# Optimization experiments

Measured on AMD Instinct MI355X. Metric: run time of the kernel, lower is better.

## Reference

```python
import jax, jax.numpy as jnp
import numpy as np

N_EMBD = 1024
N_HEAD = 16
HEAD_SIZE = N_EMBD // N_HEAD  # 64
ROT = HEAD_SIZE // 2          # 32 (int(head_size * 0.5))
BASE = 10000.0


def rotate_half(x):
    x1, x2 = x[..., : x.shape[-1] // 2], x[..., x.shape[-1] // 2 :]
    return jnp.concatenate((-x2, x1), axis=-1)


def rope_tables(T, dtype=jnp.float32):
    inv_freq = 1.0 / (BASE ** (jnp.arange(0, ROT, 2, dtype=jnp.float32) / ROT))
    t = jnp.arange(T, dtype=jnp.float32)
    freqs = jnp.einsum('i,j->ij', t, inv_freq)  # [T, ROT//2]
    emb = jnp.concatenate((freqs, freqs), axis=-1)  # [T, ROT]
    return jnp.cos(emb).astype(dtype), jnp.sin(emb).astype(dtype)


def setup_inputs() -> dict:
    key = jax.random.key(0)
    ks = jax.random.split(key, 9)
    B, T, C = 2, 2048, N_EMBD
    s = 1.0 / np.sqrt(C)
    inp = {
        'x': jax.random.normal(ks[0], (B, T, C), dtype=jnp.float32),
        'Wq': jax.random.normal(ks[1], (C, C), dtype=jnp.float32) * s,
        'bq': jnp.zeros((C,), dtype=jnp.float32),
        'Wk': jax.random.normal(ks[2], (C, C), dtype=jnp.float32) * s,
        'bk': jnp.zeros((C,), dtype=jnp.float32),
        'Wv': jax.random.normal(ks[3], (C, C), dtype=jnp.float32) * s,
        'bv': jnp.zeros((C,), dtype=jnp.float32),
        'Wo': jax.random.normal(ks[4], (C, C), dtype=jnp.float32) * s,
        'bo': jnp.zeros((C,), dtype=jnp.float32),
    }
    return inp


def reference(x, Wq, bq, Wk, bk, Wv, bv, Wo, bo):
    B, T, C = x.shape
    H, D = N_HEAD, HEAD_SIZE

    def proj(W, b):
        return (x @ W + b).reshape(B, T, H, D).transpose(0, 2, 1, 3)  # [B,H,T,D]

    q, k, v = proj(Wq, bq), proj(Wk, bk), proj(Wv, bv)

    q_rot, q_pass = q[..., :ROT], q[..., ROT:]
    k_rot, k_pass = k[..., :ROT], k[..., ROT:]
    cos, sin = rope_tables(T, x.dtype)  # [T, ROT]
    q_rot = q_rot * cos + rotate_half(q_rot) * sin
    k_rot = k_rot * cos + rotate_half(k_rot) * sin
    q = jnp.concatenate((q_rot, q_pass), axis=-1)
    k = jnp.concatenate((k_rot, k_pass), axis=-1)

    scale = 1.0 / np.sqrt(D)
    att = jnp.einsum('bhqd,bhkd->bhqk', q, k) * scale  # [B,H,T,T]
    causal = jnp.tril(jnp.ones((T, T), dtype=bool))
    att = jnp.where(causal, att, -jnp.inf)
    att = jax.nn.softmax(att, axis=-1)
    out = jnp.einsum('bhqk,bhkd->bhqd', att, v)  # [B,H,T,D]
    out = out.transpose(0, 2, 1, 3).reshape(B, T, C)
    return out @ Wo + bo
```

## Files before the change

### kernel.cpp

```cpp
#include <hip/hip_runtime.h>
#include <cstdint>
#include <cstddef>
#include <math.h>

typedef _Float16 half8 __attribute__((ext_vector_type(8)));
typedef _Float16 half4 __attribute__((ext_vector_type(4)));
typedef float f32x4 __attribute__((ext_vector_type(4)));
typedef float f32x16 __attribute__((ext_vector_type(16)));
typedef unsigned int uint2v __attribute__((ext_vector_type(2)));

#define NB  2
#define NT  2048
#define NC  1024
#define NH  16
#define ND  64

__device__ __forceinline__ void gload_lds16(const _Float16* g, _Float16* l) {
  __builtin_amdgcn_global_load_lds((const __attribute__((address_space(1))) void*)g,
                                   (__attribute__((address_space(3))) void*)l, 16, 0, 0);
}

__device__ __forceinline__ uint2v plswap(unsigned a, unsigned b) {
  return __builtin_amdgcn_permlane32_swap(a, b, false, false);
}

__global__ void k_cvt_x(const float* __restrict__ x, _Float16* __restrict__ xh) {
  const int n4 = (4096 * 1024) / 4;
  int i = blockIdx.x * 256 + threadIdx.x;
  for (; i < n4; i += 2048 * 256) {
    float4 v = ((const float4*)x)[i];
    half4 h = { (_Float16)v.x, (_Float16)v.y, (_Float16)v.z, (_Float16)v.w };
    ((half4*)xh)[i] = h;
  }
}

__global__ void k_tw(const float* __restrict__ W0, const float* __restrict__ W1,
                     const float* __restrict__ W2, const float* __restrict__ W3,
                     _Float16* __restrict__ WT) {
  const float* W = (blockIdx.z == 0) ? W0 : (blockIdx.z == 1) ? W1 : (blockIdx.z == 2) ? W2 : W3;
  _Float16* out = WT + ((size_t)blockIdx.z << 20);
  __shared__ float t[32][33];
  const int x0 = blockIdx.x * 32;
  const int y0 = blockIdx.y * 32;
  const int tx = threadIdx.x, ty = threadIdx.y;
#pragma unroll
  for (int r = 0; r < 4; ++r)
    t[ty + 8 * r][tx] = W[(size_t)(y0 + ty + 8 * r) * 1024 + x0 + tx];
  __syncthreads();
#pragma unroll
  for (int r = 0; r < 4; ++r)
    out[(size_t)(x0 + ty + 8 * r) * 1024 + y0 + tx] = (_Float16)t[tx][ty + 8 * r];
}

__device__ __forceinline__ void gemm_mainloop(const _Float16* __restrict__ A,
                                              const _Float16* __restrict__ Bmat,
                                              int m0, int n0,
                                              _Float16* As, _Float16* Bs,
                                              f32x4 acc[4][4]) {
  const int tid = threadIdx.x;
  const int lane = tid & 63;
  const int wid = tid >> 6;
  const int wm = wid >> 1, wn = wid & 1;
  const int c16 = lane & 15, rg = lane >> 4;

  for (int k0 = 0; k0 < 1024; k0 += 64) {
    __syncthreads();
#pragma unroll
    for (int i = 0; i < 4; ++i) {
      int e = (i * 256 + tid) * 8;
      int row = e >> 6;
      int chunk = (e & 63) >> 3;
      int scol = ((chunk ^ (row & 7)) << 3);
      gload_lds16(A + (size_t)(m0 + row) * 1024 + k0 + scol,
                  As + (size_t)(i * 256 + (wid << 6)) * 8);
      gload_lds16(Bmat + (size_t)(n0 + row) * 1024 + k0 + scol,
                  Bs + (size_t)(i * 256 + (wid << 6)) * 8);
    }
    __syncthreads();
#pragma unroll
    for (int kk = 0; kk < 2; ++kk) {
      half8 af[4], bfr[4];
#pragma unroll
      for (int mi = 0; mi < 4; ++mi) {
        int row = (wm << 6) + (mi << 4) + c16;
        int chunk = (kk << 2) + rg;
        af[mi] = *(const half8*)&As[(row << 6) + ((chunk ^ (row & 7)) << 3)];
      }
#pragma unroll
      for (int ni = 0; ni < 4; ++ni) {
        int row = (wn << 6) + (ni << 4) + c16;
        int chunk = (kk << 2) + rg;
        bfr[ni] = *(const half8*)&Bs[(row << 6) + ((chunk ^ (row & 7)) << 3)];
      }
#pragma unroll
      for (int mi = 0; mi < 4; ++mi)
#pragma unroll
        for (int ni = 0; ni < 4; ++ni)
          acc[mi][ni] = __builtin_amdgcn_mfma_f32_16x16x32_f16(af[mi], bfr[ni], acc[mi][ni], 0, 0, 0);
    }
  }
}

__global__ __launch_bounds__(256, 2) void k_qkv(const _Float16* __restrict__ xh,
                                                const _Float16* __restrict__ WT,
                                                const float* __restrict__ bq,
                                                const float* __restrict__ bk,
                                                const float* __restrict__ bv,
                                                _Float16* __restrict__ Qh,
                                                _Float16* __restrict__ Kh,
                                                _Float16* __restrict__ VT) {
  __shared__ __align__(16) _Float16 As[128 * 64];
  __shared__ __align__(16) _Float16 Bs[128 * 64];
  f32x4 acc[4][4];
#pragma unroll
  for (int i = 0; i < 4; ++i)
#pragma unroll
    for (int j = 0; j < 4; ++j) acc[i][j] = (f32x4){0.f, 0.f, 0.f, 0.f};

  const int m0 = blockIdx.y * 128;
  const int ng = blockIdx.x * 128;
  const int p = ng >> 10;
  const int n0 = ng & 1023;
  gemm_mainloop(xh, WT + ((size_t)p << 20), m0, n0, As, Bs, acc);

  const int tid = threadIdx.x, lane = tid & 63, wid = tid >> 6;
  const int wm = wid >> 1, wn = wid & 1, c16 = lane & 15, rg = lane >> 4;
  const float* bias = (p == 0) ? bq : (p == 1) ? bk : bv;
  const int nw = n0 + (wn << 6);
  const int head = nw >> 6;
  float bi[4];
#pragma unroll
  for (int ni = 0; ni < 4; ++ni) bi[ni] = bias[nw + (ni << 4) + c16];

  if (p == 2) {
#pragma unroll
    for (int mi = 0; mi < 4; ++mi) {
      int m = m0 + (wm << 6) + (mi << 4) + (rg << 2);
      int b = m >> 11, t0 = m & 2047;
#pragma unroll
      for (int ni = 0; ni < 4; ++ni) {
        half4 hv;
#pragma unroll
        for (int r = 0; r < 4; ++r) hv[r] = (_Float16)(acc[mi][ni][r] + bi[ni]);
        size_t base = ((size_t)(b * NH + head) * ND + (ni << 4) + c16) * NT + t0;
        *(half4*)&VT[base] = hv;
      }
    }
    return;
  }

  _Float16* Out = (p == 0) ? Qh : Kh;
  const float invf = exp2f((float)c16 * -0.8304820237218405f);
  const float qscale = (p == 0) ? 0.18033688011112042f : 1.0f;

#pragma unroll
  for (int mi = 0; mi < 4; ++mi) {
#pragma unroll
    for (int r = 0; r < 4; ++r) {
      int m = m0 + (wm << 6) + (mi << 4) + (rg << 2) + r;
      int b = m >> 11, t = m & 2047;
      float v0 = acc[mi][0][r] + bi[0];
      float v1 = acc[mi][1][r] + bi[1];
      float v2 = acc[mi][2][r] + bi[2];
      float v3 = acc[mi][3][r] + bi[3];
      {
        float th = (float)t * invf;
        float sn, cs;
        sincosf(th, &sn, &cs);
        float nx = v0 * cs - v1 * sn;
        v1 = v1 * cs + v0 * sn;
        v0 = nx;
      }
      size_t base = ((size_t)(b * NH + head) * NT + t) * ND;
      Out[base + 0 + c16]  = (_Float16)(v0 * qscale);
      Out[base + 16 + c16] = (_Float16)(v1 * qscale);
      Out[base + 32 + c16] = (_Float16)(v2 * qscale);
      Out[base + 48 + c16] = (_Float16)(v3 * qscale);
    }
  }
}

__global__ __launch_bounds__(256, 2) void k_attn(const _Float16* __restrict__ Qh,
                                                 const _Float16* __restrict__ Kh,
                                                 const _Float16* __restrict__ VT,
                                                 _Float16* __restrict__ Oh) {
  const int lin = blockIdx.x;
  const int xcd = lin & 7;
  const int w = lin >> 3;
  const int bh = (xcd << 2) | (w & 3);
  const int tile = 15 - (w >> 2);

  const int tid = threadIdx.x, lane = tid & 63, wid = tid >> 6;
  const int q31 = lane & 31, hi = lane >> 5;
  const size_t hb = (size_t)bh * NT * ND;
  const _Float16* Qp = Qh + hb;
  const _Float16* Kp = Kh + hb;
  const _Float16* Vp = VT + hb;
  const int b = bh >> 4, h = bh & 15;

  const int q0w = (tile << 7) + (wid << 5);
  const int qg = q0w + q31;
  const int end = q0w + 32;

  half8 qf[4];
#pragma unroll
  for (int c = 0; c < 4; ++c)
    qf[c] = *(const half8*)&Qp[(size_t)qg * ND + (c << 4) + (hi << 3)];

  f32x16 oacc0, oacc1, lacc;
#pragma unroll
  for (int r = 0; r < 16; ++r) { oacc0[r] = 0.f; oacc1[r] = 0.f; lacc[r] = 0.f; }
  float m = -INFINITY;

  half8 kA[4], kB[4], vfr[4];

#define LOADK(dst, ktv) do {                                                    \
    const _Float16* kp_ = Kp + (size_t)((ktv) + q31) * ND + (hi << 3);          \
    dst[0] = *(const half8*)(kp_);                                              \
    dst[1] = *(const half8*)(kp_ + 16);                                         \
    dst[2] = *(const half8*)(kp_ + 32);                                         \
    dst[3] = *(const half8*)(kp_ + 48);                                         \
  } while (0)

#define LOADV(ktv) do {                                                         \
    _Pragma("unroll")                                                           \
    for (int dh = 0; dh < 2; ++dh)                                              \
      _Pragma("unroll")                                                         \
      for (int ks = 0; ks < 2; ++ks)                                            \
        vfr[dh * 2 + ks] = *(const half8*)&Vp[(size_t)((dh << 5) + q31) * NT    \
                                              + (ktv) + (ks << 4) + (hi << 3)]; \
  } while (0)

#define BODY(kb, ktc) do {                                                      \
    f32x16 s;                                                                   \
    _Pragma("unroll")                                                           \
    for (int r = 0; r < 16; ++r) s[r] = 0.f;                                    \
    __builtin_amdgcn_s_setprio(1);                                              \
    _Pragma("unroll")                                                           \
    for (int c = 0; c < 4; ++c)                                                 \
      s = __builtin_amdgcn_mfma_f32_32x32x16_f16(kb[c], qf[c], s, 0, 0, 0);     \
    __builtin_amdgcn_s_setprio(0);                                              \
    if ((ktc) + 31 > q0w) {      \
      int rel = qg - (ktc) - (hi << 2);                                         \
      _Pragma("unroll")                                                         \
      for (int r = 0; r < 16; ++r) {                                            \
        int crow = (r & 3) + ((r >> 2) << 3);                                   \
        if (crow > rel) s[r] = -INFINITY;                                       \
      }                                                                         \
    }                                                                           \
       \
    float t8[8];                                                                \
    _Pragma("unroll")                                                           \
    for (int r = 0; r < 8; ++r) t8[r] = fmaxf(s[r], s[r + 8]);                  \
    _Pragma("unroll")                                                           \
    for (int r = 0; r < 4; ++r) t8[r] = fmaxf(t8[r], t8[r + 4]);                \
    float pm = fmaxf(fmaxf(t8[0], t8[1]), fmaxf(t8[2], t8[3]));                 \
    pm = fmaxf(pm, __shfl_xor(pm, 32));                                         \
    if (!__all(pm <= m + 11.54f)) {                 \
      float mn = fmaxf(m, pm);                                                  \
      float corr = exp2f(m - mn);                                               \
      m = mn;                                                                   \
      _Pragma("unroll")                                                         \
      for (int r = 0; r < 16; ++r) {                                            \
        oacc0[r] *= corr; oacc1[r] *= corr; lacc[r] *= corr;                    \
      }                                                                         \
    }                                                                           \
    _Pragma("unroll")                                                           \
    for (int r = 0; r < 16; ++r) {                                              \
      float pv = exp2f(s[r] - m);                                               \
      s[r] = pv; lacc[r] += pv;                                                 \
    }                                                                           \
     \
    unsigned pw0 = __builtin_bit_cast(unsigned, __builtin_amdgcn_cvt_pkrtz(s[0], s[1]));   \
    unsigned pw1 = __builtin_bit_cast(unsigned, __builtin_amdgcn_cvt_pkrtz(s[2], s[3]));   \
    unsigned pw2 = __builtin_bit_cast(unsigned, __builtin_amdgcn_cvt_pkrtz(s[4], s[5]));   \
    unsigned pw3 = __builtin_bit_cast(unsigned, __builtin_amdgcn_cvt_pkrtz(s[6], s[7]));   \
    unsigned pw4 = __builtin_bit_cast(unsigned, __builtin_amdgcn_cvt_pkrtz(s[8], s[9]));   \
    unsigned pw5 = __builtin_bit_cast(unsigned, __builtin_amdgcn_cvt_pkrtz(s[10], s[11])); \
    unsigned pw6 = __builtin_bit_cast(unsigned, __builtin_amdgcn_cvt_pkrtz(s[12], s[13])); \
    unsigned pw7 = __builtin_bit_cast(unsigned, __builtin_amdgcn_cvt_pkrtz(s[14], s[15])); \
    uint2v rA0 = plswap(pw0, pw2);   \
    uint2v rA1 = plswap(pw1, pw3);                      \
    uint2v rB0 = plswap(pw4, pw6);                      \
    uint2v rB1 = plswap(pw5, pw7);                      \
    uint4 ua, ub;                                                               \
    ua.x = rA0[0]; ua.y = rA1[0]; ua.z = rA0[1]; ua.w = rA1[1];                 \
    ub.x = rB0[0]; ub.y = rB1[0]; ub.z = rB0[1]; ub.w = rB1[1];                 \
    half8 pa0 = __builtin_bit_cast(half8, ua);                                  \
    half8 pa1 = __builtin_bit_cast(half8, ub);                                  \
    __builtin_amdgcn_s_setprio(1);                                              \
    oacc0 = __builtin_amdgcn_mfma_f32_32x32x16_f16(vfr[0], pa0, oacc0, 0, 0, 0); \
    oacc0 = __builtin_amdgcn_mfma_f32_32x32x16_f16(vfr[1], pa1, oacc0, 0, 0, 0); \
    oacc1 = __builtin_amdgcn_mfma_f32_32x32x16_f16(vfr[2], pa0, oacc1, 0, 0, 0); \
    oacc1 = __builtin_amdgcn_mfma_f32_32x32x16_f16(vfr[3], pa1, oacc1, 0, 0, 0); \
    __builtin_amdgcn_s_setprio(0);                                              \
  } while (0)

  int kt = 0;
  LOADK(kA, 0);
  for (;;) {
    LOADV(kt);
    if (kt + 32 < end) LOADK(kB, kt + 32);
    __builtin_amdgcn_sched_barrier(0);
    BODY(kA, kt);
    kt += 32;
    if (kt >= end) break;
    LOADV(kt);
    if (kt + 32 < end) LOADK(kA, kt + 32);
    __builtin_amdgcn_sched_barrier(0);
    BODY(kB, kt);
    kt += 32;
    if (kt >= end) break;
  }
#undef LOADK
#undef LOADV
#undef BODY

  float l8[8];
#pragma unroll
  for (int r = 0; r < 8; ++r) l8[r] = lacc[r] + lacc[r + 8];
#pragma unroll
  for (int r = 0; r < 4; ++r) l8[r] = l8[r] + l8[r + 4];
  float ls = (l8[0] + l8[1]) + (l8[2] + l8[3]);
  ls += __shfl_xor(ls, 32);
  float il = 1.f / ls;
  size_t obase = ((size_t)b * NT + qg) * NC + h * ND;
#pragma unroll
  for (int g = 0; g < 4; ++g) {
    int d0 = (g << 3) + (hi << 2);
    half4 h4, h5;
#pragma unroll
    for (int r = 0; r < 4; ++r) {
      h4[r] = (_Float16)(oacc0[(g << 2) + r] * il);
      h5[r] = (_Float16)(oacc1[(g << 2) + r] * il);
    }
    *(half4*)&Oh[obase + d0] = h4;
    *(half4*)&Oh[obase + 32 + d0] = h5;
  }
}

__global__ __launch_bounds__(256, 2) void k_out(const _Float16* __restrict__ Oh,
                                                const _Float16* __restrict__ WoT,
                                                const float* __restrict__ bo,
                                                float* __restrict__ out) {
  __shared__ __align__(16) _Float16 As[128 * 64];
  __shared__ __align__(16) _Float16 Bs[128 * 64];
  f32x4 acc[4][4];
#pragma unroll
  for (int i = 0; i < 4; ++i)
#pragma unroll
    for (int j = 0; j < 4; ++j) acc[i][j] = (f32x4){0.f, 0.f, 0.f, 0.f};

  const int m0 = blockIdx.y * 128;
  const int n0 = blockIdx.x * 128;
  gemm_mainloop(Oh, WoT, m0, n0, As, Bs, acc);

  const int tid = threadIdx.x, lane = tid & 63, wid = tid >> 6;
  const int wm = wid >> 1, wn = wid & 1, c16 = lane & 15, rg = lane >> 4;
  float bi[4];
#pragma unroll
  for (int ni = 0; ni < 4; ++ni) bi[ni] = bo[n0 + (wn << 6) + (ni << 4) + c16];
#pragma unroll
  for (int mi = 0; mi < 4; ++mi) {
#pragma unroll
    for (int r = 0; r < 4; ++r) {
      int m = m0 + (wm << 6) + (mi << 4) + (rg << 2) + r;
#pragma unroll
      for (int ni = 0; ni < 4; ++ni) {
        int n = n0 + (wn << 6) + (ni << 4) + c16;
        out[(size_t)m * NC + n] = acc[mi][ni][r] + bi[ni];
      }
    }
  }
}

extern "C" void kernel_launch(void* const* d_in, const int* in_sizes, int n_in,
                              void* d_out, int out_size, void* d_ws, size_t ws_size,
                              hipStream_t stream) {
  const float* x  = (const float*)d_in[0];
  const float* Wq = (const float*)d_in[1];
  const float* bq = (const float*)d_in[2];
  const float* Wk = (const float*)d_in[3];
  const float* bk = (const float*)d_in[4];
  const float* Wv = (const float*)d_in[5];
  const float* bv = (const float*)d_in[6];
  const float* Wo = (const float*)d_in[7];
  const float* bo = (const float*)d_in[8];
  float* out = (float*)d_out;

  char* ws = (char*)d_ws;
  _Float16* xh = (_Float16*)ws;
  _Float16* WT = (_Float16*)(ws + (8ull << 20));
  _Float16* Qh = (_Float16*)(ws + (16ull << 20));
  _Float16* Kh = (_Float16*)(ws + (24ull << 20));
  _Float16* Vt = (_Float16*)(ws + (32ull << 20));
  _Float16* Oh = (_Float16*)(ws + (40ull << 20));

  k_cvt_x<<<2048, 256, 0, stream>>>(x, xh);
  k_tw<<<dim3(32, 32, 4), dim3(32, 8), 0, stream>>>(Wq, Wk, Wv, Wo, WT);
  k_qkv<<<dim3(24, 32), 256, 0, stream>>>(xh, WT, bq, bk, bv, Qh, Kh, Vt);
  k_attn<<<512, 256, 0, stream>>>(Qh, Kh, Vt, Oh);
  k_out<<<dim3(8, 32), 256, 0, stream>>>(Oh, WT + (3ull << 20), bo, out);
}
```

Before: 151.9 us.

## Split attention KV range across two waves per query tile and merge via LDS

Each attention block now owns one 32-row query tile with two waves, each wave processing half of the causal key range (split-K flash attention), then merging partial max, sum and output through shared memory. The grid grows from 512 blocks of 4 waves to 2048 blocks of 2 waves, and the row-sum accumulator is halved by pre-adding pairs. The aim is to shorten the longest per-wave key loop and balance the causal triangle across more independent work units. In exchange it adds an LDS round trip, a block barrier and a rescale merge, and it drops the previous XCD-aware block mapping.

```diff
diff --git a/kernel.cpp b/kernel.cpp
--- a/kernel.cpp
+++ b/kernel.cpp
@@ -180,15 +180,13 @@
   }
 }
 
-__global__ __launch_bounds__(256, 2) void k_attn(const _Float16* __restrict__ Qh,
+__global__ __launch_bounds__(128, 4) void k_attn(const _Float16* __restrict__ Qh,
                                                  const _Float16* __restrict__ Kh,
                                                  const _Float16* __restrict__ VT,
                                                  _Float16* __restrict__ Oh) {
   const int lin = blockIdx.x;
-  const int xcd = lin & 7;
-  const int w = lin >> 3;
-  const int bh = (xcd << 2) | (w & 3);
-  const int tile = 15 - (w >> 2);
+  const int bh = lin & 31;
+  const int g = 63 - (lin >> 5);
 
   const int tid = threadIdx.x, lane = tid & 63, wid = tid >> 6;
   const int q31 = lane & 31, hi = lane >> 5;
@@ -198,18 +196,27 @@
   const _Float16* Vp = VT + hb;
   const int b = bh >> 4, h = bh & 15;
 
-  const int q0w = (tile << 7) + (wid << 5);
+  __shared__ float Osh[32][65];
+  __shared__ float msh[32], lsh[32];
+
+  const int q0w = g << 5;
   const int qg = q0w + q31;
-  const int end = q0w + 32;
+  const int n = g + 1;
+  const int nh2 = (n + 1) >> 1;
+  const int kt0   = (wid == 0) ? 0 : (nh2 << 5);
+  const int ktend = (wid == 0) ? (nh2 << 5) : (n << 5);
 
   half8 qf[4];
 #pragma unroll
   for (int c = 0; c < 4; ++c)
     qf[c] = *(const half8*)&Qp[(size_t)qg * ND + (c << 4) + (hi << 3)];
 
-  f32x16 oacc0, oacc1, lacc;
-#pragma unroll
-  for (int r = 0; r < 16; ++r) { oacc0[r] = 0.f; oacc1[r] = 0.f; lacc[r] = 0.f; }
+  f32x16 oacc0, oacc1;
+#pragma unroll
+  for (int r = 0; r < 16; ++r) { oacc0[r] = 0.f; oacc1[r] = 0.f; }
+  float lacc[8];
+#pragma unroll
+  for (int r = 0; r < 8; ++r) lacc[r] = 0.f;
   float m = -INFINITY;
 
   half8 kA[4], kB[4], vfr[4];
@@ -240,7 +247,7 @@
     for (int c = 0; c < 4; ++c)                                                 \
       s = __builtin_amdgcn_mfma_f32_32x32x16_f16(kb[c], qf[c], s, 0, 0, 0);     \
     __builtin_amdgcn_s_setprio(0);                                              \
-    if ((ktc) + 31 > q0w) {      \
+    if ((ktc) + 31 > q0w) {       \
       int rel = qg - (ktc) - (hi << 2);                                         \
       _Pragma("unroll")                                                         \
       for (int r = 0; r < 16; ++r) {                                            \
@@ -248,7 +255,7 @@
         if (crow > rel) s[r] = -INFINITY;                                       \
       }                                                                         \
     }                                                                           \
-       \
+                       \
     float t8[8];                                                                \
     _Pragma("unroll")                                                           \
     for (int r = 0; r < 8; ++r) t8[r] = fmaxf(s[r], s[r + 8]);                  \
@@ -261,16 +268,18 @@
       float corr = exp2f(m - mn);                                               \
       m = mn;                                                                   \
       _Pragma("unroll")                                                         \
-      for (int r = 0; r < 16; ++r) {                                            \
-        oacc0[r] *= corr; oacc1[r] *= corr; lacc[r] *= corr;                    \
-      }                                                                         \
+      for (int r = 0; r < 16; ++r) { oacc0[r] *= corr; oacc1[r] *= corr; }      \
+      _Pragma("unroll")                                                         \
+      for (int r = 0; r < 8; ++r) lacc[r] *= corr;                              \
     }                                                                           \
     _Pragma("unroll")                                                           \
     for (int r = 0; r < 16; ++r) {                                              \
       float pv = exp2f(s[r] - m);                                               \
-      s[r] = pv; lacc[r] += pv;                                                 \
+      s[r] = pv;                                                                \
     }                                                                           \
-     \
+    _Pragma("unroll")                                                           \
+    for (int r = 0; r < 8; ++r) lacc[r] += s[r] + s[r + 8];                     \
+      \
     unsigned pw0 = __builtin_bit_cast(unsigned, __builtin_amdgcn_cvt_pkrtz(s[0], s[1]));   \
     unsigned pw1 = __builtin_bit_cast(unsigned, __builtin_amdgcn_cvt_pkrtz(s[2], s[3]));   \
     unsigned pw2 = __builtin_bit_cast(unsigned, __builtin_amdgcn_cvt_pkrtz(s[4], s[5]));   \
@@ -279,10 +288,10 @@
     unsigned pw5 = __builtin_bit_cast(unsigned, __builtin_amdgcn_cvt_pkrtz(s[10], s[11])); \
     unsigned pw6 = __builtin_bit_cast(unsigned, __builtin_amdgcn_cvt_pkrtz(s[12], s[13])); \
     unsigned pw7 = __builtin_bit_cast(unsigned, __builtin_amdgcn_cvt_pkrtz(s[14], s[15])); \
-    uint2v rA0 = plswap(pw0, pw2);   \
-    uint2v rA1 = plswap(pw1, pw3);                      \
-    uint2v rB0 = plswap(pw4, pw6);                      \
-    uint2v rB1 = plswap(pw5, pw7);                      \
+    uint2v rA0 = plswap(pw0, pw2);                                              \
+    uint2v rA1 = plswap(pw1, pw3);                                              \
+    uint2v rB0 = plswap(pw4, pw6);                                              \
+    uint2v rB1 = plswap(pw5, pw7);                                              \
     uint4 ua, ub;                                                               \
     ua.x = rA0[0]; ua.y = rA1[0]; ua.z = rA0[1]; ua.w = rA1[1];                 \
     ub.x = rB0[0]; ub.y = rB1[0]; ub.z = rB0[1]; ub.w = rB1[1];                 \
@@ -296,46 +305,66 @@
     __builtin_amdgcn_s_setprio(0);                                              \
   } while (0)
 
-  int kt = 0;
-  LOADK(kA, 0);
-  for (;;) {
-    LOADV(kt);
-    if (kt + 32 < end) LOADK(kB, kt + 32);
-    __builtin_amdgcn_sched_barrier(0);
-    BODY(kA, kt);
-    kt += 32;
-    if (kt >= end) break;
-    LOADV(kt);
-    if (kt + 32 < end) LOADK(kA, kt + 32);
-    __builtin_amdgcn_sched_barrier(0);
-    BODY(kB, kt);
-    kt += 32;
-    if (kt >= end) break;
+  int kt = kt0;
+  if (kt < ktend) {
+    LOADK(kA, kt);
+    for (;;) {
+      LOADV(kt);
+      if (kt + 32 < ktend) LOADK(kB, kt + 32);
+      __builtin_amdgcn_sched_barrier(0);
+      BODY(kA, kt);
+      kt += 32;
+      if (kt >= ktend) break;
+      LOADV(kt);
+      if (kt + 32 < ktend) LOADK(kA, kt + 32);
+      __builtin_amdgcn_sched_barrier(0);
+      BODY(kB, kt);
+      kt += 32;
+      if (kt >= ktend) break;
+    }
   }
 #undef LOADK
 #undef LOADV
 #undef BODY
 
-  float l8[8];
-#pragma unroll
-  for (int r = 0; r < 8; ++r) l8[r] = lacc[r] + lacc[r + 8];
-#pragma unroll
-  for (int r = 0; r < 4; ++r) l8[r] = l8[r] + l8[r + 4];
-  float ls = (l8[0] + l8[1]) + (l8[2] + l8[3]);
+  float l4[4];
+#pragma unroll
+  for (int r = 0; r < 4; ++r) l4[r] = lacc[r] + lacc[r + 4];
+  float ls = (l4[0] + l4[1]) + (l4[2] + l4[3]);
   ls += __shfl_xor(ls, 32);
-  float il = 1.f / ls;
-  size_t obase = ((size_t)b * NT + qg) * NC + h * ND;
-#pragma unroll
-  for (int g = 0; g < 4; ++g) {
-    int d0 = (g << 3) + (hi << 2);
-    half4 h4, h5;
-#pragma unroll
-    for (int r = 0; r < 4; ++r) {
-      h4[r] = (_Float16)(oacc0[(g << 2) + r] * il);
-      h5[r] = (_Float16)(oacc1[(g << 2) + r] * il);
-    }
-    *(half4*)&Oh[obase + d0] = h4;
-    *(half4*)&Oh[obase + 32 + d0] = h5;
+
+  if (wid == 1) {
+    if (hi == 0) { msh[q31] = m; lsh[q31] = ls; }
+#pragma unroll
+    for (int g2 = 0; g2 < 4; ++g2)
+#pragma unroll
+      for (int r = 0; r < 4; ++r) {
+        int d0 = (g2 << 3) + (hi << 2) + r;
+        Osh[q31][d0] = oacc0[(g2 << 2) + r];
+        Osh[q31][32 + d0] = oacc1[(g2 << 2) + r];
+      }
+  }
+  __syncthreads();
+  if (wid == 0) {
+    float m1 = msh[q31], l1 = lsh[q31];
+    float M = fmaxf(m, m1);
+    float c0 = exp2f(m - M);
+    float c1 = exp2f(m1 - M);
+    float lt = c0 * ls + c1 * l1;
+    float il = 1.f / lt;
+    size_t obase = ((size_t)b * NT + qg) * NC + h * ND;
+#pragma unroll
+    for (int g2 = 0; g2 < 4; ++g2) {
+      int d0 = (g2 << 3) + (hi << 2);
+      half4 h4, h5;
+#pragma unroll
+      for (int r = 0; r < 4; ++r) {
+        h4[r] = (_Float16)((c0 * oacc0[(g2 << 2) + r] + c1 * Osh[q31][d0 + r]) * il);
+        h5[r] = (_Float16)((c0 * oacc1[(g2 << 2) + r] + c1 * Osh[q31][32 + d0 + r]) * il);
+      }
+      *(half4*)&Oh[obase + d0] = h4;
+      *(half4*)&Oh[obase + 32 + d0] = h5;
+    }
   }
 }
 
@@ -399,6 +428,6 @@
   k_cvt_x<<<2048, 256, 0, stream>>>(x, xh);
   k_tw<<<dim3(32, 32, 4), dim3(32, 8), 0, stream>>>(Wq, Wk, Wv, Wo, WT);
   k_qkv<<<dim3(24, 32), 256, 0, stream>>>(xh, WT, bq, bk, bv, Qh, Kh, Vt);
-  k_attn<<<512, 256, 0, stream>>>(Qh, Kh, Vt, Oh);
+  k_attn<<<2048, 128, 0, stream>>>(Qh, Kh, Vt, Oh);
   k_out<<<dim3(8, 32), 256, 0, stream>>>(Oh, WT + (3ull << 20), bo, out);
 }
```

Result: slower. 243.0 us (+60.0%).
